# Optimization experiments

Hardware: AMD Instinct MI355X
Metric: run time of the kernel (lower is better)

## Reference

```python
import jax, jax.numpy as jnp
import numpy as np
from jax import lax

T, B, E = 512, 128, 128  # timesteps, batch, embedding_size
S = 2 * T                # stack capacity: 2 pushes per step


def setup_inputs() -> dict:
    key = jax.random.key(0)
    k1, k2, k3, k4, k5 = jax.random.split(key, 5)
    return {
        "v1": jax.random.normal(k1, (T, B, E), dtype=jnp.float32),
        "v2": jax.random.normal(k2, (T, B, E), dtype=jnp.float32),
        "d1": jax.random.uniform(k3, (T, B, 1), dtype=jnp.float32),
        "d2": jax.random.uniform(k4, (T, B, 1), dtype=jnp.float32),
        "u": jax.random.uniform(k5, (T, B, 1), dtype=jnp.float32),
    }


def _step(carry, xs):
    strengths, values = carry  # [B,S], [B,S,E]; slots 0..2(t+1)-1 valid after push
    v1t, v2t, d1t, d2t, ut, t = xs  # v*: [B,E]; d*,u: [B,1]; t: scalar int
    # --- push: append two entries at the top (slots 2t, 2t+1) ---
    values = lax.dynamic_update_slice(
        values, jnp.stack([v1t, v2t], axis=1), (0, 2 * t, 0))
    strengths = lax.dynamic_update_slice(
        strengths, jnp.concatenate([d1t, d2t], axis=1), (0, 2 * t))
    # exclusive reverse cumsum = strength used above each slot (top-down order)
    rev_incl = jnp.flip(jnp.cumsum(jnp.flip(strengths, 1), axis=1), 1)  # [B,S]
    used = rev_incl - strengths  # [B,S]
    # --- read: faithful to torch.max(u - strength_used) reducing over batch ---
    m = jnp.max(ut - used, axis=0)            # [S] scalar-over-batch per slot
    w = jnp.minimum(strengths, m[None, :])    # [B,S]; invalid slots hit v=0
    summary = jnp.einsum('bs,bse->be', w, values)  # [B,E]
    # --- pop: s -= min(s, relu(u - used)) using pre-pop strengths ---
    pop_amt = jnp.minimum(strengths, jnp.maximum(0.0, ut - used))
    strengths = strengths - pop_amt
    return (strengths, values), summary


def reference(v1, v2, d1, d2, u):
    init = (jnp.zeros((B, S), v1.dtype), jnp.zeros((B, S, E), v1.dtype))
    ts = jnp.arange(T, dtype=jnp.int32)
    _, out = lax.scan(_step, init, (v1, v2, d1, d2, u, ts))
    return out  # [T,B,E]: read content at each timestep
```

## Files before the change

### kernel.cpp

```cpp
#include <hip/hip_runtime.h>
#include <cstdint>
#include <cstddef>

#define TT 512
#define BB 128
#define EE 128
#define SS 1024
#define NEG_INF (-1e30f)

typedef _Float16 half8 __attribute__((ext_vector_type(8)));
typedef float floatx4 __attribute__((ext_vector_type(4)));

__device__ __forceinline__ unsigned int pkh(float x, float y) {
    _Float16 hx = (_Float16)x, hy = (_Float16)y;
    unsigned short bx, by;
    __builtin_memcpy(&bx, &hx, 2); __builtin_memcpy(&by, &hy, 2);
    return (unsigned int)bx | ((unsigned int)by << 16);
}

__global__ __launch_bounds__(64) void prefixF(
    const float* __restrict__ d1, const float* __restrict__ d2,
    const float* __restrict__ u,
    float* __restrict__ F, float* __restrict__ Bv,
    float* __restrict__ d2T, float* __restrict__ FT,
    float* __restrict__ BvT, float* __restrict__ CST,
    float* __restrict__ CMT, float* __restrict__ HT,
    float* __restrict__ CSb)
{
    const int b = blockIdx.x;
    const int lane = threadIdx.x;
    const int t0 = lane * 8;

    float l1[8], l2[8], g[8];
#pragma unroll
    for (int j = 0; j < 8; ++j) {
        const int t = t0 + j;
        l1[j] = d1[t * BB + b];
        l2[j] = d2[t * BB + b];
        g[j] = u[t * BB + b] - l1[j] - l2[j];
    }
    float p[8], s = 0.f;
#pragma unroll
    for (int j = 0; j < 8; ++j) { s += g[j]; p[j] = s; }

    float v = s;
#pragma unroll
    for (int off = 1; off < 64; off <<= 1) {
        float o = __shfl_up(v, off);
        if (lane >= off) v += o;
    }
    const float excl = v - s;

    float Fv[8];
#pragma unroll
    for (int j = 0; j < 8; ++j) Fv[j] = excl + p[j];

#pragma unroll
    for (int j = 0; j < 8; ++j) {
        const int t = t0 + j;
        const float Fm1 = (j > 0) ? Fv[j - 1] : excl;
        const float Bvv = Fm1 - l1[j];
        F  [b * TT + t] = Fv[j];
        Bv [b * TT + t] = Bvv;
        d2T[b * TT + t] = l2[j];
        FT [t * BB + b] = Fv[j];
        BvT[t * BB + b] = Bvv;
    }

    float pm[8], sm[8];
    pm[0] = Fv[0];
#pragma unroll
    for (int j = 1; j < 8; ++j) pm[j] = fmaxf(pm[j - 1], Fv[j]);
    sm[7] = Fv[7];
#pragma unroll
    for (int j = 6; j >= 0; --j) sm[j] = fmaxf(sm[j + 1], Fv[j]);

    float pcar = NEG_INF, scar = NEG_INF;
#pragma unroll
    for (int off = 1; off <= 3; ++off) {
        float xu = __shfl_up(pm[7], off);
        if ((lane & 3) >= off) pcar = fmaxf(pcar, xu);
        float xd = __shfl_down(sm[0], off);
        if ((lane & 3) + off <= 3) scar = fmaxf(scar, xd);
    }

#pragma unroll
    for (int j = 0; j < 8; ++j) {
        const int t = t0 + j;
        const float Hv  = fmaxf(pcar, (j > 0) ? pm[j - 1] : NEG_INF);
        const float CSv = fmaxf(sm[j], scar);
        HT [t * BB + b] = Hv;
        CST[t * BB + b] = CSv;
        CSb[b * TT + t] = CSv;
    }
    if ((lane & 3) == 0)
        CMT[(lane >> 2) * BB + b] = fmaxf(sm[0], scar);
}

__global__ __launch_bounds__(256) void calcM2(
    const float* __restrict__ FT, const float* __restrict__ BvT,
    const float* __restrict__ CST, const float* __restrict__ CMT,
    const float* __restrict__ HT, const float* __restrict__ u,
    float* __restrict__ m)
{
    const int t = (int)blockIdx.y;
    const int ci = (int)blockIdx.x;
    const int ct = t >> 5;
    if (ci > ct) return;

    const int tid = threadIdx.x;
    const int b = tid & 127, h = tid >> 7;
    const int ib = 32 * ci;

    __shared__ float cand[BB][66];
    __shared__ float Tot[2][BB];
    __shared__ float red[4][64];

    const float Ft = FT[t * BB + b];

    if (ci < ct) {
        float K = HT[t * BB + b];
        for (int c = ci + 1; c < ct; ++c) K = fmaxf(K, CMT[c * BB + b]);
#pragma unroll
        for (int j = 0; j < 16; ++j) {
            const int jj = 16 * h + j;
            const int i = ib + jj;
            const float R = fmaxf(CST[i * BB + b], K);
            const float Bvv = BvT[i * BB + b];
            cand[b][2 * jj]     = Ft - fmaxf(Bvv, R);
            cand[b][2 * jj + 1] = Ft - R;
        }
    } else {
        float vv[16], sfx[16];
#pragma unroll
        for (int j = 0; j < 16; ++j) {
            const int i = ib + 16 * h + j;
            vv[j] = (i < t) ? FT[i * BB + b] : NEG_INF;
        }
        sfx[15] = vv[15];
#pragma unroll
        for (int j = 14; j >= 0; --j) sfx[j] = fmaxf(vv[j], sfx[j + 1]);
        Tot[h][b] = sfx[0];
        __syncthreads();
        const float carry = (h == 0) ? Tot[1][b] : NEG_INF;
        const float ub = u[t * BB + b];
#pragma unroll
        for (int j = 0; j < 16; ++j) {
            const int jj = 16 * h + j;
            const int i = ib + jj;
            const float R = fmaxf(sfx[j], carry);
            const float Bvv = BvT[i * BB + b];
            cand[b][2 * jj]     = Ft - fmaxf(Bvv, R);
            cand[b][2 * jj + 1] = (i == t) ? ub : (Ft - R);
        }
    }
    __syncthreads();

    {
        const int s = tid & 63, g = tid >> 6;
        float mx = NEG_INF;
        const int b0 = g * 32;
#pragma unroll 8
        for (int bb = b0; bb < b0 + 32; ++bb) mx = fmaxf(mx, cand[bb][s]);
        red[g][s] = mx;
    }
    __syncthreads();
    if (tid < 64) {
        const float r = fmaxf(fmaxf(red[0][tid], red[1][tid]),
                              fmaxf(red[2][tid], red[3][tid]));
        const int s_glob = 64 * ci + tid;
        if (s_glob < 2 * t + 2) m[(size_t)t * SS + s_glob] = r;
    }
}

#define PWH 72
#define PWW 36
#define VTO 2304
#define TPO 6912
#define FT0O 6976
#define SCMO 7040

__global__ __launch_bounds__(256) void phaseC_mfma(
    const float* __restrict__ F, const float* __restrict__ Bvg,
    const float* __restrict__ d2T, const float* __restrict__ CSb,
    const float* __restrict__ CMT, const float* __restrict__ m,
    const float* __restrict__ v1, const float* __restrict__ v2,
    float* __restrict__ out)
{
    const int b  = blockIdx.x & (BB - 1);
    const int wk = blockIdx.x >> 7;

    int tt, ck0, nck;
    if (wk < 6) {
        nck = 8;
        ck0 = (wk == 1) ? 8 : 0;
        tt  = (wk <= 1) ? 7 : 8 - wk;
    } else {
        const int j = wk - 6;
        nck = 6 - 2 * (j >> 1);
        if (j & 1) { tt = 2 - (j >> 1); ck0 = 0; }
        else       { tt = 6 - (j >> 1); ck0 = 8; }
    }
    const int t0 = tt * 64;
    const int t0c = t0 >> 5;
    const int ckEnd = ck0 + nck;
    const bool splitTile = (tt >= 4);

    const int tid = threadIdx.x;

    __shared__ float sh[7056];

    const int lane = tid & 63, w = tid >> 6;
    const int wr = w >> 1, wc = w & 1;
    const int n = lane & 15;
    const int kq = (lane >> 4) * 8;
    const int il = tid & 31, g = tid >> 5;
    const int veb = tid & 7;
    const int vip = ((tid >> 3) & 7) + 8 * wc;
    const int veh = wr * 64;

    float4 pv[8];
    float2 pmv[8];
    float pAi, pBi, pAux;

    auto prefetch = [&](int ck) {
        const int i = 32 * ck + il;
#pragma unroll
        for (int r8 = 0; r8 < 8; ++r8) {
            const int t = t0 + 8 * g + r8;
            pmv[r8] = *(const float2*)&m[(size_t)t * SS + 2 * i];
        }
        pAi  = F  [b * TT + ((i > 0) ? i - 1 : 0)];
        pBi  = Bvg[b * TT + i];
        pAux = (32 * ck < t0) ? CSb[b * TT + i] : d2T[b * TT + i];
        const int i0 = 32 * ck + 2 * vip, i1 = i0 + 1;
        const float* p10 = v1 + ((size_t)i0 * BB + b) * EE;
        const float* p11 = v1 + ((size_t)i1 * BB + b) * EE;
        const float* p20 = v2 + ((size_t)i0 * BB + b) * EE;
        const float* p21 = v2 + ((size_t)i1 * BB + b) * EE;
#pragma unroll
        for (int c = 0; c < 2; ++c) {
            const int e0 = 4 * veb + 32 * c + veh;
            pv[4 * c + 0] = *(const float4*)&p10[e0];
            pv[4 * c + 1] = *(const float4*)&p11[e0];
            pv[4 * c + 2] = *(const float4*)&p20[e0];
            pv[4 * c + 3] = *(const float4*)&p21[e0];
        }
    };

    if (tid < 64) {
        float xi = F[b * TT + t0 + tid];
        sh[FT0O + tid] = xi;
        float sc = xi;
#pragma unroll
        for (int off = 1; off < 64; off <<= 1) {
            const float y = __shfl_up(sc, off);
            if (tid >= off) sc = fmaxf(sc, y);
        }
        const float ex = __shfl_up(sc, 1);
        sh[TPO + tid] = (tid == 0) ? NEG_INF : ex;
    } else if (tid < 128) {
        const int c = tid - 64;
        float cm = (c < t0c) ? CMT[c * BB + b] : NEG_INF;
#pragma unroll
        for (int off = 1; off < 16; off <<= 1) {
            const float y = __shfl_down(cm, off);
            cm = fmaxf(cm, (c + off < 16) ? y : NEG_INF);
        }
        if (c < 16) sh[SCMO + c] = cm;
    }

    prefetch(ck0);

    __syncthreads();

    float Freg2[8];
#pragma unroll
    for (int j = 0; j < 8; ++j) Freg2[j] = sh[FT0O + 8 * g + j];
    const float qstart = sh[TPO + 8 * g];

    floatx4 acc[2][4];
#pragma unroll
    for (int r = 0; r < 2; ++r)
#pragma unroll
        for (int j = 0; j < 4; ++j) acc[r][j] = (floatx4)0.f;

    for (int ck = ck0; ck < ckEnd; ++ck) {
        const int ib = 32 * ck;
        const int i = ib + il;
        const bool below = (ib < t0);

        uint2 vreg[8];
#pragma unroll
        for (int c = 0; c < 2; ++c) {
            const float4 xa = pv[4 * c + 0], xb = pv[4 * c + 1];
            const float4 ya = pv[4 * c + 2], yb = pv[4 * c + 3];
            vreg[4 * c + 0] = make_uint2(pkh(xa.x, ya.x), pkh(xb.x, yb.x));
            vreg[4 * c + 1] = make_uint2(pkh(xa.y, ya.y), pkh(xb.y, yb.y));
            vreg[4 * c + 2] = make_uint2(pkh(xa.z, ya.z), pkh(xb.z, yb.z));
            vreg[4 * c + 3] = make_uint2(pkh(xa.w, ya.w), pkh(xb.w, yb.w));
        }

        unsigned int wreg[8];
        {
            const float Ai = (i > 0) ? pAi : 0.f;
            const float Bi = pBi;
            const int li = i - t0;
            float q, S0i = 0.f;
            if (below) {
                S0i = fmaxf(pAux, sh[SCMO + ck + 1]);
                q = qstart;
            } else {
                q = NEG_INF;
                for (int k = li; k < 8 * g; ++k)
                    q = fmaxf(q, sh[FT0O + k]);
            }
#pragma unroll
            for (int r8 = 0; r8 < 8; ++r8) {
                const int t_l = 8 * g + r8;
                const float2 mv = pmv[r8];
                float w0 = 0.f, w1 = 0.f;
                if (below) {
                    const float R = fmaxf(S0i, q);
                    const float a0 = fmaxf(Ai, R) - fmaxf(Bi, R);
                    const float a1 = fmaxf(Bi - R, 0.f);
                    w0 = fminf(a0, mv.x);
                    w1 = fminf(a1, mv.y);
                    q = fmaxf(q, Freg2[r8]);
                } else {
                    if (li <= t_l) {
                        const float R = q;
                        const float a0 = fmaxf(Ai, R) - fmaxf(Bi, R);
                        const float a1 = (li == t_l) ? pAux
                                                     : fmaxf(Bi - R, 0.f);
                        w0 = fminf(a0, mv.x);
                        w1 = fminf(a1, mv.y);
                    }
                    q = fmaxf(q, (t_l >= li) ? Freg2[r8] : NEG_INF);
                }
                wreg[r8] = pkh(w0, w1);
            }
        }

        __syncthreads();

#pragma unroll
        for (int r8 = 0; r8 < 8; ++r8)
            ((unsigned int*)sh)[(8 * g + r8) * PWW + il] = wreg[r8];
        {
            unsigned int* vt = (unsigned int*)sh + VTO;
            const int dw = 2 * vip;
#pragma unroll
            for (int c = 0; c < 2; ++c) {
                const int e0 = 4 * veb + 32 * c + veh;
                *(uint2*)&vt[(e0 + 0) * PWW + dw] = vreg[4 * c + 0];
                *(uint2*)&vt[(e0 + 1) * PWW + dw] = vreg[4 * c + 1];
                *(uint2*)&vt[(e0 + 2) * PWW + dw] = vreg[4 * c + 2];
                *(uint2*)&vt[(e0 + 3) * PWW + dw] = vreg[4 * c + 3];
            }
        }

        __syncthreads();

        if (ck + 1 < ckEnd) prefetch(ck + 1);

        __builtin_amdgcn_s_setprio(1);
        {
            const _Float16* WsH = (const _Float16*)sh;
            const _Float16* VtH = (const _Float16*)(sh + VTO);
#pragma unroll
            for (int k2 = 0; k2 < 64; k2 += 32) {
                const half8 av0 = *(const half8*)&WsH[(32 * wr + n) * PWH + kq + k2];
                const half8 av1 = *(const half8*)&WsH[(32 * wr + 16 + n) * PWH + kq + k2];
#pragma unroll
                for (int j = 0; j < 4; ++j) {
                    const half8 bv = *(const half8*)&VtH[(64 * wc + 16 * j + n) * PWH + kq + k2];
                    acc[0][j] = __builtin_amdgcn_mfma_f32_16x16x32_f16(av0, bv, acc[0][j], 0, 0, 0);
                    acc[1][j] = __builtin_amdgcn_mfma_f32_16x16x32_f16(av1, bv, acc[1][j], 0, 0, 0);
                }
            }
        }
        __builtin_amdgcn_s_setprio(0);
    }

    {
        const int q = lane >> 4;
#pragma unroll
        for (int r = 0; r < 2; ++r) {
#pragma unroll
            for (int j = 0; j < 4; ++j) {
#pragma unroll
                for (int reg = 0; reg < 4; ++reg) {
                    const int t = t0 + 32 * wr + 16 * r + 4 * q + reg;
                    const int col = 64 * wc + 16 * j + n;
                    float* dst = &out[((size_t)t * BB + b) * EE + col];
                    if (splitTile) atomicAdd(dst, acc[r][j][reg]);
                    else           *dst = acc[r][j][reg];
                }
            }
        }
    }
}

extern "C" void kernel_launch(void* const* d_in, const int* in_sizes, int n_in,
                              void* d_out, int out_size, void* d_ws, size_t ws_size,
                              hipStream_t stream) {
    const float* v1 = (const float*)d_in[0];
    const float* v2 = (const float*)d_in[1];
    const float* d1 = (const float*)d_in[2];
    const float* d2 = (const float*)d_in[3];
    const float* u  = (const float*)d_in[4];
    float* out = (float*)d_out;

    char* ws = (char*)d_ws;
    float* m   = (float*)ws;
    float* F   = m   + (size_t)TT * SS;
    float* Bvp = F   + (size_t)BB * TT;
    float* d2T = Bvp + (size_t)BB * TT;
    float* FT  = d2T + (size_t)BB * TT;
    float* BvT = FT  + (size_t)BB * TT;
    float* CST = BvT + (size_t)BB * TT;
    float* HT  = CST + (size_t)BB * TT;
    float* CMT = HT  + (size_t)BB * TT;
    float* CSb = CMT + (size_t)16 * BB;

    hipMemsetAsync(out + (size_t)256 * BB * EE, 0,
                   (size_t)256 * BB * EE * sizeof(float), stream);

    prefixF<<<dim3(BB), dim3(64), 0, stream>>>(d1, d2, u, F, Bvp, d2T, FT,
                                               BvT, CST, CMT, HT, CSb);
    calcM2 <<<dim3(16, TT), dim3(256), 0, stream>>>(FT, BvT, CST, CMT, HT, u, m);
    phaseC_mfma<<<dim3(12 * BB), dim3(256), 0, stream>>>(F, Bvp, d2T, CSb, CMT,
                                                         m, v1, v2, out);
}
```

Before: 206.5 us.

## Double-buffer LDS staging in phaseC and drop split-tile atomics

```diff
diff --git a/kernel.cpp b/kernel.cpp
--- a/kernel.cpp
+++ b/kernel.cpp
@@ -173,12 +173,13 @@
     }
 }
 
-#define PWH 72
-#define PWW 36
-#define VTO 2304
-#define TPO 6912
-#define FT0O 6976
-#define SCMO 7040
+#define BUFW 6144
+#define BUFH 12288
+#define VTW  2048
+#define VTH  4096
+#define FT0O 12288
+#define TPO  12352
+#define SCMO 12416
 
 __global__ __launch_bounds__(256) void phaseC_mfma(
     const float* __restrict__ F, const float* __restrict__ Bvg,
@@ -188,27 +189,14 @@
     float* __restrict__ out)
 {
     const int b  = blockIdx.x & (BB - 1);
-    const int wk = blockIdx.x >> 7;
-
-    int tt, ck0, nck;
-    if (wk < 6) {
-        nck = 8;
-        ck0 = (wk == 1) ? 8 : 0;
-        tt  = (wk <= 1) ? 7 : 8 - wk;
-    } else {
-        const int j = wk - 6;
-        nck = 6 - 2 * (j >> 1);
-        if (j & 1) { tt = 2 - (j >> 1); ck0 = 0; }
-        else       { tt = 6 - (j >> 1); ck0 = 8; }
-    }
+    const int tt = 7 - (blockIdx.x >> 7);
     const int t0 = tt * 64;
     const int t0c = t0 >> 5;
-    const int ckEnd = ck0 + nck;
-    const bool splitTile = (tt >= 4);
+    const int nchunks = 2 * tt + 2;
 
     const int tid = threadIdx.x;
 
-    __shared__ float sh[7056];
+    __shared__ float sh[12432];
 
     const int lane = tid & 63, w = tid >> 6;
     const int wr = w >> 1, wc = w & 1;
@@ -248,67 +236,22 @@
         }
     };
 
-    if (tid < 64) {
-        float xi = F[b * TT + t0 + tid];
-        sh[FT0O + tid] = xi;
-        float sc = xi;
-#pragma unroll
-        for (int off = 1; off < 64; off <<= 1) {
-            const float y = __shfl_up(sc, off);
-            if (tid >= off) sc = fmaxf(sc, y);
-        }
-        const float ex = __shfl_up(sc, 1);
-        sh[TPO + tid] = (tid == 0) ? NEG_INF : ex;
-    } else if (tid < 128) {
-        const int c = tid - 64;
-        float cm = (c < t0c) ? CMT[c * BB + b] : NEG_INF;
-#pragma unroll
-        for (int off = 1; off < 16; off <<= 1) {
-            const float y = __shfl_down(cm, off);
-            cm = fmaxf(cm, (c + off < 16) ? y : NEG_INF);
-        }
-        if (c < 16) sh[SCMO + c] = cm;
-    }
-
-    prefetch(ck0);
-
-    __syncthreads();
-
     float Freg2[8];
-#pragma unroll
-    for (int j = 0; j < 8; ++j) Freg2[j] = sh[FT0O + 8 * g + j];
-    const float qstart = sh[TPO + 8 * g];
-
-    floatx4 acc[2][4];
-#pragma unroll
-    for (int r = 0; r < 2; ++r)
-#pragma unroll
-        for (int j = 0; j < 4; ++j) acc[r][j] = (floatx4)0.f;
-
-    for (int ck = ck0; ck < ckEnd; ++ck) {
-        const int ib = 32 * ck;
-        const int i = ib + il;
-        const bool below = (ib < t0);
-
-        uint2 vreg[8];
-#pragma unroll
-        for (int c = 0; c < 2; ++c) {
-            const float4 xa = pv[4 * c + 0], xb = pv[4 * c + 1];
-            const float4 ya = pv[4 * c + 2], yb = pv[4 * c + 3];
-            vreg[4 * c + 0] = make_uint2(pkh(xa.x, ya.x), pkh(xb.x, yb.x));
-            vreg[4 * c + 1] = make_uint2(pkh(xa.y, ya.y), pkh(xb.y, yb.y));
-            vreg[4 * c + 2] = make_uint2(pkh(xa.z, ya.z), pkh(xb.z, yb.z));
-            vreg[4 * c + 3] = make_uint2(pkh(xa.w, ya.w), pkh(xb.w, yb.w));
-        }
+    float qstart;
+
+    auto stage = [&](int cks) {
+        const int iS = 32 * cks + il;
+        const bool belowS = (32 * cks < t0);
+        const int p = cks & 1;
 
         unsigned int wreg[8];
         {
-            const float Ai = (i > 0) ? pAi : 0.f;
+            const float Ai = (iS > 0) ? pAi : 0.f;
             const float Bi = pBi;
-            const int li = i - t0;
+            const int li = iS - t0;
             float q, S0i = 0.f;
-            if (below) {
-                S0i = fmaxf(pAux, sh[SCMO + ck + 1]);
+            if (belowS) {
+                S0i = fmaxf(pAux, sh[SCMO + cks + 1]);
                 q = qstart;
             } else {
                 q = NEG_INF;
@@ -320,7 +263,7 @@
                 const int t_l = 8 * g + r8;
                 const float2 mv = pmv[r8];
                 float w0 = 0.f, w1 = 0.f;
-                if (below) {
+                if (belowS) {
                     const float R = fmaxf(S0i, q);
                     const float a0 = fmaxf(Ai, R) - fmaxf(Bi, R);
                     const float a1 = fmaxf(Bi - R, 0.f);
@@ -342,45 +285,104 @@
             }
         }
 
-        __syncthreads();
+        uint2 vreg[8];
+#pragma unroll
+        for (int c = 0; c < 2; ++c) {
+            const float4 xa = pv[4 * c + 0], xb = pv[4 * c + 1];
+            const float4 ya = pv[4 * c + 2], yb = pv[4 * c + 3];
+            vreg[4 * c + 0] = make_uint2(pkh(xa.x, ya.x), pkh(xb.x, yb.x));
+            vreg[4 * c + 1] = make_uint2(pkh(xa.y, ya.y), pkh(xb.y, yb.y));
+            vreg[4 * c + 2] = make_uint2(pkh(xa.z, ya.z), pkh(xb.z, yb.z));
+            vreg[4 * c + 3] = make_uint2(pkh(xa.w, ya.w), pkh(xb.w, yb.w));
+        }
 
 #pragma unroll
         for (int r8 = 0; r8 < 8; ++r8)
-            ((unsigned int*)sh)[(8 * g + r8) * PWW + il] = wreg[r8];
+            ((unsigned int*)sh)[p * BUFW + (8 * g + r8) * 32 + (il ^ (r8 << 2))]
+                = wreg[r8];
         {
-            unsigned int* vt = (unsigned int*)sh + VTO;
-            const int dw = 2 * vip;
+            unsigned int* vt = (unsigned int*)sh + p * BUFW + VTW;
 #pragma unroll
             for (int c = 0; c < 2; ++c) {
                 const int e0 = 4 * veb + 32 * c + veh;
-                *(uint2*)&vt[(e0 + 0) * PWW + dw] = vreg[4 * c + 0];
-                *(uint2*)&vt[(e0 + 1) * PWW + dw] = vreg[4 * c + 1];
-                *(uint2*)&vt[(e0 + 2) * PWW + dw] = vreg[4 * c + 2];
-                *(uint2*)&vt[(e0 + 3) * PWW + dw] = vreg[4 * c + 3];
-            }
-        }
-
-        __syncthreads();
-
-        if (ck + 1 < ckEnd) prefetch(ck + 1);
-
-        __builtin_amdgcn_s_setprio(1);
-        {
-            const _Float16* WsH = (const _Float16*)sh;
-            const _Float16* VtH = (const _Float16*)(sh + VTO);
-#pragma unroll
-            for (int k2 = 0; k2 < 64; k2 += 32) {
-                const half8 av0 = *(const half8*)&WsH[(32 * wr + n) * PWH + kq + k2];
-                const half8 av1 = *(const half8*)&WsH[(32 * wr + 16 + n) * PWH + kq + k2];
-#pragma unroll
-                for (int j = 0; j < 4; ++j) {
-                    const half8 bv = *(const half8*)&VtH[(64 * wc + 16 * j + n) * PWH + kq + k2];
-                    acc[0][j] = __builtin_amdgcn_mfma_f32_16x16x32_f16(av0, bv, acc[0][j], 0, 0, 0);
-                    acc[1][j] = __builtin_amdgcn_mfma_f32_16x16x32_f16(av1, bv, acc[1][j], 0, 0, 0);
+#pragma unroll
+                for (int k = 0; k < 4; ++k) {
+                    const int e = e0 + k;
+                    *(uint2*)&vt[e * 32 + ((2 * vip) ^ ((e & 7) << 2))]
+                        = vreg[4 * c + k];
                 }
             }
         }
+    };
+
+    floatx4 acc[2][4];
+#pragma unroll
+    for (int r = 0; r < 2; ++r)
+#pragma unroll
+        for (int j = 0; j < 4; ++j) acc[r][j] = (floatx4)0.f;
+
+    auto mfma_step = [&](int ck) {
+        const int p = ck & 1;
+        const _Float16* base = (const _Float16*)sh + p * BUFH;
+        const int xsw = (n & 7) << 3;
+        __builtin_amdgcn_s_setprio(1);
+#pragma unroll
+        for (int k2 = 0; k2 < 64; k2 += 32) {
+            const int colr = (kq + k2) ^ xsw;
+            const half8 av0 = *(const half8*)&base[(32 * wr + n) * 64 + colr];
+            const half8 av1 = *(const half8*)&base[(32 * wr + 16 + n) * 64 + colr];
+#pragma unroll
+            for (int j = 0; j < 4; ++j) {
+                const half8 bv = *(const half8*)&base[VTH +
+                                     (64 * wc + 16 * j + n) * 64 + colr];
+                acc[0][j] = __builtin_amdgcn_mfma_f32_16x16x32_f16(av0, bv, acc[0][j], 0, 0, 0);
+                acc[1][j] = __builtin_amdgcn_mfma_f32_16x16x32_f16(av1, bv, acc[1][j], 0, 0, 0);
+            }
+        }
         __builtin_amdgcn_s_setprio(0);
+    };
+
+    prefetch(0);
+
+    if (tid < 64) {
+        float xi = F[b * TT + t0 + tid];
+        sh[FT0O + tid] = xi;
+        float sc = xi;
+#pragma unroll
+        for (int off = 1; off < 64; off <<= 1) {
+            const float y = __shfl_up(sc, off);
+            if (tid >= off) sc = fmaxf(sc, y);
+        }
+        const float ex = __shfl_up(sc, 1);
+        sh[TPO + tid] = (tid == 0) ? NEG_INF : ex;
+    } else if (tid < 128) {
+        const int c = tid - 64;
+        float cm = (c < t0c) ? CMT[c * BB + b] : NEG_INF;
+#pragma unroll
+        for (int off = 1; off < 16; off <<= 1) {
+            const float y = __shfl_down(cm, off);
+            cm = fmaxf(cm, (c + off < 16) ? y : NEG_INF);
+        }
+        if (c < 16) sh[SCMO + c] = cm;
+    }
+
+    __syncthreads();
+
+#pragma unroll
+    for (int j = 0; j < 8; ++j) Freg2[j] = sh[FT0O + 8 * g + j];
+    qstart = sh[TPO + 8 * g];
+
+    stage(0);
+    if (1 < nchunks) prefetch(1);
+    __syncthreads();
+
+    for (int ck = 0; ck < nchunks; ++ck) {
+        mfma_step(ck);
+        if (ck + 1 < nchunks) {
+            stage(ck + 1);
+            if (ck + 2 < nchunks) prefetch(ck + 2);
+        }
+        __syncthreads();
     }
 
     {
@@ -393,9 +395,7 @@
                 for (int reg = 0; reg < 4; ++reg) {
                     const int t = t0 + 32 * wr + 16 * r + 4 * q + reg;
                     const int col = 64 * wc + 16 * j + n;
-                    float* dst = &out[((size_t)t * BB + b) * EE + col];
-                    if (splitTile) atomicAdd(dst, acc[r][j][reg]);
-                    else           *dst = acc[r][j][reg];
+                    out[((size_t)t * BB + b) * EE + col] = acc[r][j][reg];
                 }
             }
         }
@@ -424,12 +424,9 @@
     float* CMT = HT  + (size_t)BB * TT;
     float* CSb = CMT + (size_t)16 * BB;
 
-    hipMemsetAsync(out + (size_t)256 * BB * EE, 0,
-                   (size_t)256 * BB * EE * sizeof(float), stream);
-
     prefixF<<<dim3(BB), dim3(64), 0, stream>>>(d1, d2, u, F, Bvp, d2T, FT,
                                                BvT, CST, CMT, HT, CSb);
     calcM2 <<<dim3(16, TT), dim3(256), 0, stream>>>(FT, BvT, CST, CMT, HT, u, m);
-    phaseC_mfma<<<dim3(12 * BB), dim3(256), 0, stream>>>(F, Bvp, d2T, CSb, CMT,
-                                                         m, v1, v2, out);
+    phaseC_mfma<<<dim3(8 * BB), dim3(256), 0, stream>>>(F, Bvp, d2T, CSb, CMT,
+                                                        m, v1, v2, out);
 }
```

Result: faster. 186.3 us (-9.8%).
